# Optimization experiments

Hardware: AMD Instinct MI355X
Metric: run time of the kernel (lower is better)

The kernel has to match this reference:

```python
import jax, jax.numpy as jnp
import numpy as np

L1_PENALTY = 0.01
RHO = 5.0
N_ITERS = 100  # fixed iteration count standing in for max_iter=2000 w/ tol
EPS = 1e-12


def _normalize(x):
    # matches torch.nn.functional.normalize(dim=1, eps=1e-12)
    n = jnp.linalg.norm(x, axis=-1, keepdims=True)
    return x / jnp.maximum(n, EPS)


def _admm_nnlasso(D, Y, lam, rho, n_iters):
    """Batched nonnegative Lasso via ADMM.
    Solves per-row: min_w 0.5*||D^T w - y||^2 + lam*||w||_1, w >= 0.
    D: [c, d] dictionary, Y: [B, d] targets. Returns W: [B, c].
    x-update uses Woodbury: (A^T A + rho I)^{-1} b = (b - A^T (G + rho I)^{-1} A b)/rho
    with A = D^T, G = A A^T = D^T D ([d, d], d=512 -> cheap Cholesky).
    """
    d = D.shape[1]
    G = D.T @ D + rho * jnp.eye(d, dtype=D.dtype)  # [d, d]
    cf = jax.scipy.linalg.cho_factor(G)
    Aty = Y @ D.T  # [B, c] = A^T y batched
    thr = lam / rho

    def step(carry, _):
        z, u = carry
        b = Aty + rho * (z - u)               # [B, c]
        s = jax.scipy.linalg.cho_solve(cf, (b @ D).T).T  # [B, d]
        x = (b - s @ D.T) / rho               # [B, c]
        z_new = jnp.maximum(x + u - thr, 0.0)  # nonneg soft-threshold
        u_new = u + x - z_new
        return (z_new, u_new), None

    z0 = jnp.zeros_like(Aty)
    (z, _), _ = jax.lax.scan(step, (z0, z0), None, length=n_iters)
    return z


def setup_inputs() -> dict:
    key = jax.random.key(0)
    k1, k2, k3, k4 = jax.random.split(key, 4)
    B, C, Dm = 1024, 10000, 512
    image = jax.random.normal(k1, (B, Dm), dtype=jnp.float32)
    text = jax.random.normal(k2, (B, Dm), dtype=jnp.float32)
    image_mean = 0.1 * jax.random.normal(k3, (Dm,), dtype=jnp.float32)
    dictionary = jax.random.normal(k4, (C, Dm), dtype=jnp.float32)
    dictionary = dictionary / jnp.linalg.norm(dictionary, axis=1, keepdims=True)
    return {"image": image, "text": text, "image_mean": image_mean,
            "dictionary": dictionary}


def reference(image, text, image_mean, dictionary):
    # encode_image
    img = _normalize(image)
    centered = _normalize(img - image_mean)
    weights = _admm_nnlasso(dictionary, centered, L1_PENALTY, RHO, N_ITERS)
    recon = weights @ dictionary           # [B, d]
    recon = _normalize(recon)
    recon = _normalize(recon + image_mean)
    # encode_text (decomp_text=False -> just normalize)
    txt = _normalize(text)
    return recon, txt
```

## Files before the change

### kernel.cpp

```cpp
#include <hip/hip_runtime.h>
#include <cstddef>
#include <cstdint>

#define BDIM  1024
#define DM    512
#define CREAL 10000
#define CP    10112
#define KSPL  16
#define RHOC  5.0f
#define THRC  (0.01f/5.0f)
#define NIT   100
#define NSIT  12

typedef float f32x4 __attribute__((ext_vector_type(4)));
typedef _Float16 f16x8 __attribute__((ext_vector_type(8)));
typedef _Float16 f16x4 __attribute__((ext_vector_type(4)));
typedef unsigned int u32x4 __attribute__((ext_vector_type(4)));


__device__ __forceinline__ f16x8 scl6(f16x8 v) {
    f16x8 r;
#pragma unroll
    for (int i = 0; i < 8; i++) r[i] = v[i] * (_Float16)0.015625f;
    return r;
}

__device__ __forceinline__ void absfold(f16x8& h8, f16x8& l8) {
    u32x4 h = __builtin_bit_cast(u32x4, h8);
    u32x4 l = __builtin_bit_cast(u32x4, l8);
    u32x4 m = h & 0x80008000u;
    h8 = __builtin_bit_cast(f16x8, h ^ m);
    l8 = __builtin_bit_cast(f16x8, l ^ m);
}

__device__ __forceinline__ void relufold(f16x8& h8, f16x8& l8) {
#pragma unroll
    for (int e = 0; e < 8; e++) {
        bool p = h8[e] > (_Float16)0;
        if (!p) { h8[e] = (_Float16)0; l8[e] = (_Float16)0; }
    }
}

__device__ __forceinline__ size_t psidx(int row, int col) {
    return ((size_t)(row >> 4) * (CP >> 5) + (size_t)(col >> 5)) * 512
         + (size_t)((((col >> 3) & 3) * 16 + (row & 15)) * 8 + (col & 7));
}

__device__ __forceinline__ void dma16(const _Float16* g, _Float16* l) {
    __builtin_amdgcn_global_load_lds(
        (const __attribute__((address_space(1))) void*)g,
        (__attribute__((address_space(3))) void*)l, 16, 0, 0);
}

__device__ __forceinline__ float blk_sum256(float v) {
    __shared__ float sb[4];
#pragma unroll
    for (int o = 32; o; o >>= 1) v += __shfl_down(v, o, 64);
    int lane = threadIdx.x & 63, w = threadIdx.x >> 6;
    __syncthreads();
    if (lane == 0) sb[w] = v;
    __syncthreads();
    return sb[0] + sb[1] + sb[2] + sb[3];
}

__global__ __launch_bounds__(256) void knorm_rows(const float* __restrict__ X,
                                                  float* __restrict__ out) {
    int row = blockIdx.x, t = threadIdx.x;
    int off = row * DM + t * 2;
    float2 v = *(const float2*)(X + off);
    float ss = blk_sum256(v.x * v.x + v.y * v.y);
    float inv = 1.0f / fmaxf(sqrtf(ss), 1e-12f);
    float2 o = {v.x * inv, v.y * inv};
    *(float2*)(out + off) = o;
}

__global__ __launch_bounds__(256) void kprep_Y(const float* __restrict__ img,
                                               const float* __restrict__ mean,
                                               float* __restrict__ Y) {
    int row = blockIdx.x, t = threadIdx.x;
    int off = row * DM + t * 2;
    float2 v = *(const float2*)(img + off);
    float ss = blk_sum256(v.x * v.x + v.y * v.y);
    float inv = 1.0f / fmaxf(sqrtf(ss), 1e-12f);
    float2 mm = *(const float2*)(mean + t * 2);
    float tx = v.x * inv - mm.x, ty = v.y * inv - mm.y;
    float ss2 = blk_sum256(tx * tx + ty * ty);
    float inv2 = 1.0f / fmaxf(sqrtf(ss2), 1e-12f);
    float2 o = {tx * inv2, ty * inv2};
    *(float2*)(Y + off) = o;
}

__global__ __launch_bounds__(256) void ktrs(const float* __restrict__ in,
                                            float* __restrict__ out32,
                                            _Float16* __restrict__ oH,
                                            _Float16* __restrict__ oL,
                                            int Rvalid, int Cin, int Rout) {
    __shared__ float tile[64][65];
    int r0 = blockIdx.x * 64;
    int c0 = blockIdx.y * 64;
    int t = threadIdx.x;
    int ri = r0 + (t >> 2);
    int cc = (t & 3) * 16;
#pragma unroll
    for (int q = 0; q < 4; ++q) {
        float4 v = {0.f, 0.f, 0.f, 0.f};
        if (ri < Rvalid) v = *(const float4*)(in + (size_t)ri * Cin + c0 + cc + q * 4);
        *(float4*)&tile[t >> 2][cc + q * 4] = v;
    }
    __syncthreads();
    int oc = c0 + (t >> 2);
    int orr = r0 + (t & 3) * 16;
    _Float16 hv[16], lv[16];
#pragma unroll
    for (int q = 0; q < 16; ++q) {
        float v = tile[(t & 3) * 16 + q][t >> 2];
        _Float16 h = (_Float16)v;
        _Float16 l = (_Float16)((v - (float)h) * 64.f);
        hv[q] = h; lv[q] = l;
        if (out32) out32[(size_t)oc * Rout + orr + q] = (float)h + (float)l * 0.015625f;
    }
    int rt = oc >> 4, rin = oc & 15;
    int kt = orr >> 5;
    int kq0 = (orr >> 3) & 3;
    size_t base = ((size_t)rt * (Rout >> 5) + kt) * 512;
    *(f16x8*)(oH + base + (size_t)(kq0 * 16 + rin) * 8)       = *(f16x8*)&hv[0];
    *(f16x8*)(oH + base + (size_t)((kq0 + 1) * 16 + rin) * 8) = *(f16x8*)&hv[8];
    *(f16x8*)(oL + base + (size_t)(kq0 * 16 + rin) * 8)       = *(f16x8*)&lv[0];
    *(f16x8*)(oL + base + (size_t)((kq0 + 1) * 16 + rin) * 8) = *(f16x8*)&lv[8];
}

__global__ void kcsum(const float* __restrict__ Dt, float* __restrict__ csum) {
    int n = blockIdx.x, t = threadIdx.x;
    float s = 0.f;
    for (int k = t; k < CP; k += 64) s += Dt[(size_t)n * CP + k];
#pragma unroll
    for (int o = 32; o; o >>= 1) s += __shfl_down(s, o, 64);
    if (t == 0) csum[n] = s;
}

__global__ __launch_bounds__(256) void kG(const float* __restrict__ Dt,
                                          float* __restrict__ G) {
    __shared__ float As[32][68];
    __shared__ float Bs[32][68];
    int tid = threadIdx.x;
    int j0 = blockIdx.x * 64, i0 = blockIdx.y * 64;
    int tn = (tid & 15) * 4, tm = (tid >> 4) * 4;
    float acc[4][4];
#pragma unroll
    for (int i = 0; i < 4; i++)
#pragma unroll
        for (int j = 0; j < 4; j++) acc[i][j] = 0.f;
    for (int k0 = 0; k0 < CP; k0 += 32) {
        __syncthreads();
#pragma unroll
        for (int p = 0; p < 2; ++p) {
            int idx = tid + p * 256;
            int row = idx >> 3, kv = (idx & 7) << 2;
            float4 va = *(const float4*)(Dt + (size_t)(i0 + row) * CP + k0 + kv);
            As[kv + 0][row] = va.x; As[kv + 1][row] = va.y;
            As[kv + 2][row] = va.z; As[kv + 3][row] = va.w;
            float4 vb = *(const float4*)(Dt + (size_t)(j0 + row) * CP + k0 + kv);
            Bs[kv + 0][row] = vb.x; Bs[kv + 1][row] = vb.y;
            Bs[kv + 2][row] = vb.z; Bs[kv + 3][row] = vb.w;
        }
        __syncthreads();
#pragma unroll
        for (int k = 0; k < 32; ++k) {
            float4 a4 = *(const float4*)&As[k][tm];
            float4 b4 = *(const float4*)&Bs[k][tn];
            float af[4] = {a4.x, a4.y, a4.z, a4.w};
            float bf[4] = {b4.x, b4.y, b4.z, b4.w};
#pragma unroll
            for (int i = 0; i < 4; i++)
#pragma unroll
                for (int j = 0; j < 4; j++) acc[i][j] = fmaf(af[i], bf[j], acc[i][j]);
        }
    }
#pragma unroll
    for (int i = 0; i < 4; i++)
#pragma unroll
        for (int j = 0; j < 4; j++) {
            int gi = i0 + tm + i, gj = j0 + tn + j;
            G[gi * DM + gj] = acc[i][j] + ((gi == gj) ? RHOC : 0.f);
        }
}

__global__ void krow_abssum(const float* __restrict__ G, float* __restrict__ gmax) {
    int row = blockIdx.x, t = threadIdx.x;
    float s = 0.f;
    for (int j = t; j < DM; j += 64) s += fabsf(G[row * DM + j]);
#pragma unroll
    for (int o = 32; o; o >>= 1) s += __shfl_down(s, o, 64);
    if (t == 0) atomicMax((int*)gmax, __float_as_int(s));
}

__global__ void kinit_X0(const float* __restrict__ gmax, float* __restrict__ X) {
    int idx = blockIdx.x * 256 + threadIdx.x;
    int i = idx >> 9, j = idx & 511;
    X[idx] = (i == j) ? (1.0f / gmax[0]) : 0.0f;
}

__global__ __launch_bounds__(256) void kgemm_ns_T(const float* __restrict__ G,
                                                  const float* __restrict__ X,
                                                  float* __restrict__ T) {
    __shared__ float As[32][68];
    __shared__ float Bs[32][68];
    int tid = threadIdx.x;
    int n0 = blockIdx.x * 64, m0 = blockIdx.y * 64;
    int tn = (tid & 15) * 4, tm = (tid >> 4) * 4;
    float acc[4][4];
#pragma unroll
    for (int i = 0; i < 4; i++)
#pragma unroll
        for (int j = 0; j < 4; j++) acc[i][j] = 0.f;
    for (int k0 = 0; k0 < DM; k0 += 32) {
        __syncthreads();
#pragma unroll
        for (int p = 0; p < 2; ++p) {
            int idx = tid + p * 256;
            {
                int row = idx >> 3, kv = (idx & 7) << 2;
                float4 v = *(const float4*)(G + (m0 + row) * DM + k0 + kv);
                As[kv + 0][row] = v.x; As[kv + 1][row] = v.y;
                As[kv + 2][row] = v.z; As[kv + 3][row] = v.w;
            }
            {
                int r = idx >> 4, cv = (idx & 15) << 2;
                *(float4*)&Bs[r][cv] = *(const float4*)(X + (k0 + r) * DM + n0 + cv);
            }
        }
        __syncthreads();
#pragma unroll
        for (int k = 0; k < 32; ++k) {
            float4 a4 = *(const float4*)&As[k][tm];
            float4 b4 = *(const float4*)&Bs[k][tn];
            float af[4] = {a4.x, a4.y, a4.z, a4.w};
            float bf[4] = {b4.x, b4.y, b4.z, b4.w};
#pragma unroll
            for (int i = 0; i < 4; i++)
#pragma unroll
                for (int j = 0; j < 4; j++) acc[i][j] = fmaf(af[i], bf[j], acc[i][j]);
        }
    }
#pragma unroll
    for (int i = 0; i < 4; i++) {
        float4 o = {acc[i][0], acc[i][1], acc[i][2], acc[i][3]};
        *(float4*)(T + (m0 + tm + i) * DM + n0 + tn) = o;
    }
}

__global__ __launch_bounds__(256) void kgemm_ns_X(const float* __restrict__ Xo,
                                                  const float* __restrict__ T,
                                                  float* __restrict__ Xn) {
    __shared__ float As[32][68];
    __shared__ float Bs[32][68];
    int tid = threadIdx.x;
    int n0 = blockIdx.x * 64, m0 = blockIdx.y * 64;
    int tn = (tid & 15) * 4, tm = (tid >> 4) * 4;
    float acc[4][4];
#pragma unroll
    for (int i = 0; i < 4; i++)
#pragma unroll
        for (int j = 0; j < 4; j++) acc[i][j] = 0.f;
    for (int k0 = 0; k0 < DM; k0 += 32) {
        __syncthreads();
#pragma unroll
        for (int p = 0; p < 2; ++p) {
            int idx = tid + p * 256;
            {
                int row = idx >> 3, kv = (idx & 7) << 2;
                float4 v = *(const float4*)(Xo + (m0 + row) * DM + k0 + kv);
                As[kv + 0][row] = v.x; As[kv + 1][row] = v.y;
                As[kv + 2][row] = v.z; As[kv + 3][row] = v.w;
            }
            {
                int r = idx >> 4, cv = (idx & 15) << 2;
                *(float4*)&Bs[r][cv] = *(const float4*)(T + (k0 + r) * DM + n0 + cv);
            }
        }
        __syncthreads();
#pragma unroll
        for (int k = 0; k < 32; ++k) {
            float4 a4 = *(const float4*)&As[k][tm];
            float4 b4 = *(const float4*)&Bs[k][tn];
            float af[4] = {a4.x, a4.y, a4.z, a4.w};
            float bf[4] = {b4.x, b4.y, b4.z, b4.w};
#pragma unroll
            for (int i = 0; i < 4; i++)
#pragma unroll
                for (int j = 0; j < 4; j++) acc[i][j] = fmaf(af[i], bf[j], acc[i][j]);
        }
    }
#pragma unroll
    for (int i = 0; i < 4; i++) {
        int base = (m0 + tm + i) * DM + n0 + tn;
        float4 xo = *(const float4*)(Xo + base);
        float4 o = {2.f * xo.x - acc[i][0], 2.f * xo.y - acc[i][1],
                    2.f * xo.z - acc[i][2], 2.f * xo.w - acc[i][3]};
        *(float4*)(Xn + base) = o;
    }
}

template <int MODE>
__global__ __launch_bounds__(256) void kgemm_nn64(const float* __restrict__ A,
                                                  const float* __restrict__ B,
                                                  float* __restrict__ out32,
                                                  _Float16* __restrict__ oA) {
    __shared__ float As[32][68];
    __shared__ float Bs[32][68];
    int tid = threadIdx.x;
    int n0 = blockIdx.x * 64, m0 = blockIdx.y * 64;
    int tn = (tid & 15) * 4, tm = (tid >> 4) * 4;
    float acc[4][4];
#pragma unroll
    for (int i = 0; i < 4; i++)
#pragma unroll
        for (int j = 0; j < 4; j++) acc[i][j] = 0.f;
    for (int k0 = 0; k0 < DM; k0 += 32) {
        __syncthreads();
#pragma unroll
        for (int p = 0; p < 2; ++p) {
            int idx = tid + p * 256;
            {
                int row = idx >> 3, kv = (idx & 7) << 2;
                float4 v = *(const float4*)(A + (size_t)(m0 + row) * DM + k0 + kv);
                As[kv + 0][row] = v.x; As[kv + 1][row] = v.y;
                As[kv + 2][row] = v.z; As[kv + 3][row] = v.w;
            }
            {
                int r = idx >> 4, cv = (idx & 15) << 2;
                *(float4*)&Bs[r][cv] = *(const float4*)(B + (size_t)(k0 + r) * CP + n0 + cv);
            }
        }
        __syncthreads();
#pragma unroll
        for (int k = 0; k < 32; ++k) {
            float4 a4 = *(const float4*)&As[k][tm];
            float4 b4 = *(const float4*)&Bs[k][tn];
            float af[4] = {a4.x, a4.y, a4.z, a4.w};
            float bf[4] = {b4.x, b4.y, b4.z, b4.w};
#pragma unroll
            for (int i = 0; i < 4; i++)
#pragma unroll
                for (int j = 0; j < 4; j++) acc[i][j] = fmaf(af[i], bf[j], acc[i][j]);
        }
    }
#pragma unroll
    for (int i = 0; i < 4; i++)
#pragma unroll
        for (int j = 0; j < 4; j++) {
            size_t idx = (size_t)(m0 + tm + i) * CP + n0 + tn + j;
            if (MODE == 0) out32[idx] = acc[i][j];
            else           oA[idx] = (_Float16)(acc[i][j] * 0.2f * 64.f);
        }
}

__global__ __launch_bounds__(256) void kgemm_aD(const float* __restrict__ Yb,
                                                const float* __restrict__ G,
                                                const float* __restrict__ csum,
                                                float* __restrict__ aD) {
    __shared__ float As[32][68];
    __shared__ float Bs[32][68];
    int tid = threadIdx.x;
    int n0 = blockIdx.x * 64, m0 = blockIdx.y * 64;
    int tn = (tid & 15) * 4, tm = (tid >> 4) * 4;
    float acc[4][4];
#pragma unroll
    for (int i = 0; i < 4; i++)
#pragma unroll
        for (int j = 0; j < 4; j++) acc[i][j] = 0.f;
    for (int k0 = 0; k0 < DM; k0 += 32) {
        __syncthreads();
#pragma unroll
        for (int p = 0; p < 2; ++p) {
            int idx = tid + p * 256;
            {
                int row = idx >> 3, kv = (idx & 7) << 2;
                float4 v = *(const float4*)(Yb + (size_t)(m0 + row) * DM + k0 + kv);
                As[kv + 0][row] = v.x; As[kv + 1][row] = v.y;
                As[kv + 2][row] = v.z; As[kv + 3][row] = v.w;
            }
            {
                int r = idx >> 4, cv = (idx & 15) << 2;
                *(float4*)&Bs[r][cv] = *(const float4*)(G + (k0 + r) * DM + n0 + cv);
            }
        }
        __syncthreads();
#pragma unroll
        for (int k = 0; k < 32; ++k) {
            float4 a4 = *(const float4*)&As[k][tm];
            float4 b4 = *(const float4*)&Bs[k][tn];
            float af[4] = {a4.x, a4.y, a4.z, a4.w};
            float bf[4] = {b4.x, b4.y, b4.z, b4.w};
#pragma unroll
            for (int i = 0; i < 4; i++)
#pragma unroll
                for (int j = 0; j < 4; j++) acc[i][j] = fmaf(af[i], bf[j], acc[i][j]);
        }
    }
    float4 c4 = *(const float4*)(csum + n0 + tn);
#pragma unroll
    for (int i = 0; i < 4; i++) {
        int base = (m0 + tm + i) * DM + n0 + tn;
        float4 y4 = *(const float4*)(Yb + base);
        float4 o = {acc[i][0] * 0.2f - y4.x - THRC * c4.x,
                    acc[i][1] * 0.2f - y4.y - THRC * c4.y,
                    acc[i][2] * 0.2f - y4.z - THRC * c4.z,
                    acc[i][3] * 0.2f - y4.w - THRC * c4.w};
        *(float4*)(aD + base) = o;
    }
}

__global__ void kinit_s(_Float16* __restrict__ SHp, _Float16* __restrict__ SLp) {
    size_t i = ((size_t)blockIdx.x * 256 + threadIdx.x) * 8;
    _Float16 h = (_Float16)(-THRC);
    _Float16 l = (_Float16)((-THRC - (float)h) * 64.f);
    f16x8 hv, lv;
#pragma unroll
    for (int e = 0; e < 8; e++) { hv[e] = h; lv[e] = l; }
    *(f16x8*)(SHp + i) = hv;
    *(f16x8*)(SLp + i) = lv;
}


__device__ __forceinline__ void stage2(_Float16* __restrict__ sab,
                                       const _Float16* __restrict__ AHp,
                                       const _Float16* __restrict__ ALp,
                                       const _Float16* __restrict__ BHp,
                                       const _Float16* __restrict__ BLp,
                                       int sp, int mtbB, int ntbB, int ktA, int ktB,
                                       int wvu, int lane) {
#pragma unroll
    for (int k = 0; k < 4; ++k) {
        const int c = wvu * 4 + k;
        const int t = (c >> 1) & 7;
        const int p = c & 1;
        const _Float16* gp;
        if (c < 16) gp = (p ? ALp : AHp) + ((size_t)(mtbB + t) * ktA + sp) * 512 + (size_t)lane * 8;
        else        gp = (p ? BLp : BHp) + ((size_t)(ntbB + t) * ktB + sp) * 512 + (size_t)lane * 8;
        dma16(gp, sab + (size_t)c * 512);
    }
}

template <int FOLD>
__device__ __forceinline__ void compute8(const _Float16* __restrict__ sab,
                                         int wm, int wn, int lane,
                                         f32x4 (&acc)[4][2]) {
    const int ta = wm >> 4;
    const int tb = wn >> 4;
    f16x8 bh[2], bl[2], bs_[2];
#pragma unroll
    for (int j = 0; j < 2; ++j) {
        const _Float16* p = sab + 8192 + (size_t)(tb + j) * 1024 + (size_t)lane * 8;
        bh[j] = *(const f16x8*)p;
        bl[j] = *(const f16x8*)(p + 512);
        bs_[j] = scl6(bh[j]);
    }
    f16x8 ah[4], al[4], as_[4];
#pragma unroll
    for (int i = 0; i < 4; ++i) {
        const _Float16* p = sab + (size_t)(ta + i) * 1024 + (size_t)lane * 8;
        ah[i] = *(const f16x8*)p;
        al[i] = *(const f16x8*)(p + 512);
    }
#pragma unroll
    for (int i = 0; i < 4; ++i) {
        if (FOLD == 0) absfold(ah[i], al[i]);
        else if (FOLD == 1) relufold(ah[i], al[i]);
        as_[i] = scl6(ah[i]);
    }
#pragma unroll
    for (int i = 0; i < 4; ++i)
#pragma unroll
        for (int j = 0; j < 2; ++j) {
            acc[i][j] = __builtin_amdgcn_mfma_f32_16x16x32_f16(ah[i],  bh[j], acc[i][j], 0, 0, 0);
            acc[i][j] = __builtin_amdgcn_mfma_f32_16x16x32_f16(as_[i], bl[j], acc[i][j], 0, 0, 0);
            acc[i][j] = __builtin_amdgcn_mfma_f32_16x16x32_f16(al[i],  bs_[j], acc[i][j], 0, 0, 0);
        }
}

template <int MODE>
__global__ __launch_bounds__(512, 4) void kg1f(const _Float16* __restrict__ SHp,
                                               const _Float16* __restrict__ SLp,
                                               const _Float16* __restrict__ DHs,
                                               const _Float16* __restrict__ DLs,
                                               float* __restrict__ Qp) {
    __shared__ _Float16 sAB[2][16384];
    const int raw = blockIdx.x;
    const int xcd = raw & 7;
    const int r   = raw >> 3;
    const int ks  = xcd * 2 + (r & 1);
    const int q   = r >> 1;
    const int mb  = q >> 2, nb = q & 3;
    const int n0 = nb * 128, m0 = mb * 128;
    const int tid = threadIdx.x;
    const int lane = tid & 63;
    const int wvu = tid >> 6;
    const int wm = (wvu >> 2) * 64;
    const int wn = (wvu & 3) * 32;
    f32x4 acc[4][2] = {};

    const int steps = CP / 32;
    const int per = (steps + KSPL - 1) / KSPL;
    int s0 = ks * per;
    int s1 = s0 + per; if (s1 > steps) s1 = steps;

    const int mtbB = m0 >> 4;
    const int ntbB = n0 >> 4;
    const int KT = CP / 32;

    stage2(sAB[0], SHp, SLp, DHs, DLs, s0, mtbB, ntbB, KT, KT, wvu, lane);
    __syncthreads();

    for (int sp = s0; sp < s1; sp += 2) {
        stage2(sAB[1], SHp, SLp, DHs, DLs, sp + 1, mtbB, ntbB, KT, KT, wvu, lane);
        compute8<MODE>(sAB[0], wm, wn, lane, acc);
        __syncthreads();
        if (sp + 2 < s1)
            stage2(sAB[0], SHp, SLp, DHs, DLs, sp + 2, mtbB, ntbB, KT, KT, wvu, lane);
        compute8<MODE>(sAB[1], wm, wn, lane, acc);
        __syncthreads();
    }

    float* outp = Qp + (size_t)ks * (BDIM * DM);
    const int r0 = (lane >> 4) * 4, c0l = lane & 15;
#pragma unroll
    for (int i = 0; i < 4; i++)
#pragma unroll
        for (int v = 0; v < 4; v++) {
            int row = m0 + wm + i * 16 + r0 + v;
#pragma unroll
            for (int j = 0; j < 2; j++)
                outp[(size_t)row * DM + n0 + wn + j * 16 + c0l] = acc[i][j][v];
        }
}

template <int ADD>
__global__ void kredf(const float* __restrict__ Qp, const float* __restrict__ aD,
                      float* __restrict__ out32, _Float16* __restrict__ QH,
                      _Float16* __restrict__ QL) {
    size_t b = ((size_t)blockIdx.x * 256 + threadIdx.x) * 4;
    float4 s = {0.f, 0.f, 0.f, 0.f};
    if (ADD) s = *(const float4*)(aD + b);
#pragma unroll
    for (int qq = 0; qq < KSPL; qq++) {
        float4 t = *(const float4*)(Qp + (size_t)qq * (BDIM * DM) + b);
        s.x += t.x; s.y += t.y; s.z += t.z; s.w += t.w;
    }
    if (ADD) {
        int row = (int)(b >> 9), col = (int)(b & 511);
        size_t t0 = ((size_t)(row >> 4) * 16 + (size_t)(col >> 5)) * 512
                  + (size_t)((((col >> 3) & 3) * 16 + (row & 15)) * 8 + (col & 7));
        float sv[4] = {s.x, s.y, s.z, s.w};
        f16x4 h4, l4;
#pragma unroll
        for (int e = 0; e < 4; e++) {
            _Float16 h = (_Float16)sv[e];
            h4[e] = h;
            l4[e] = (_Float16)((sv[e] - (float)h) * 64.f);
        }
        *(f16x4*)(QH + t0) = h4;
        *(f16x4*)(QL + t0) = l4;
    } else {
        *(float4*)(out32 + b) = s;
    }
}

__global__ __launch_bounds__(512, 4) void kg2f(const _Float16* __restrict__ QH,
                                               const _Float16* __restrict__ QL,
                                               const _Float16* __restrict__ EHs,
                                               const _Float16* __restrict__ ELs,
                                               const _Float16* __restrict__ AH,
                                               _Float16* __restrict__ SHp,
                                               _Float16* __restrict__ SLp) {
    __shared__ _Float16 sAB[2][16384];
    const int raw = blockIdx.x;
    const int g = raw & 7;
    const int q = raw >> 3;
    const int mb = q & 7, jj = q >> 3;
    const int nb = g * 10 + jj;
    if (nb >= 79) return;
    const int n0 = nb * 128, m0 = mb * 128;
    const int tid = threadIdx.x;
    const int lane = tid & 63;
    const int wvu = tid >> 6;
    const int wm = (wvu >> 2) * 64;
    const int wn = (wvu & 3) * 32;
    const int mtbB = m0 >> 4;
    const int ntbB = n0 >> 4;
    const int KT = DM / 32;
    f32x4 acc[4][2] = {};

    stage2(sAB[0], QH, QL, EHs, ELs, 0, mtbB, ntbB, KT, KT, wvu, lane);
    __syncthreads();

    for (int kk = 0; kk < KT; kk += 2) {
        stage2(sAB[1], QH, QL, EHs, ELs, kk + 1, mtbB, ntbB, KT, KT, wvu, lane);
        compute8<2>(sAB[0], wm, wn, lane, acc);
        __syncthreads();
        if (kk + 2 < KT)
            stage2(sAB[0], QH, QL, EHs, ELs, kk + 2, mtbB, ntbB, KT, KT, wvu, lane);
        compute8<2>(sAB[1], wm, wn, lane, acc);
        __syncthreads();
    }

    const int r0 = (lane >> 4) * 4, c0l = lane & 15;
#pragma unroll
    for (int i = 0; i < 4; i++)
#pragma unroll
        for (int v = 0; v < 4; v++) {
            int row = m0 + wm + i * 16 + r0 + v;
#pragma unroll
            for (int j = 0; j < 2; j++) {
                int col = n0 + wn + j * 16 + c0l;
                size_t idx = (size_t)row * CP + col;
                size_t ps = psidx(row, col);
                float a = (float)AH[idx] * 0.015625f;
                float sold = (float)SHp[ps] + (float)SLp[ps] * 0.015625f;
                float z = fmaxf(sold, 0.f);
                float pn = a + z - acc[i][j][v];
                float sn = pn - THRC;
                _Float16 h = (_Float16)sn;
                SHp[ps] = h;
                SLp[ps] = (_Float16)((sn - (float)h) * 64.f);
            }
        }
}

__global__ __launch_bounds__(256) void kfinal(const float* __restrict__ Qf,
                                              const float* __restrict__ mean,
                                              float* __restrict__ out) {
    int row = blockIdx.x, t = threadIdx.x;
    int off = row * DM + t * 2;
    float2 qv = *(const float2*)(Qf + off);
    float rx = qv.x, ry = qv.y;
    float ss = blk_sum256(rx * rx + ry * ry);
    float inv = 1.0f / fmaxf(sqrtf(ss), 1e-12f);
    rx *= inv; ry *= inv;
    float2 mm = *(const float2*)(mean + t * 2);
    rx += mm.x; ry += mm.y;
    float ss2 = blk_sum256(rx * rx + ry * ry);
    float inv2 = 1.0f / fmaxf(sqrtf(ss2), 1e-12f);
    float2 o = {rx * inv2, ry * inv2};
    *(float2*)(out + off) = o;
}

extern "C" void kernel_launch(void* const* d_in, const int* in_sizes, int n_in,
                              void* d_out, int out_size, void* d_ws, size_t ws_size,
                              hipStream_t stream) {
    const float* image = (const float*)d_in[0];
    const float* text  = (const float*)d_in[1];
    const float* mean  = (const float*)d_in[2];
    const float* D     = (const float*)d_in[3];
    float* out = (float*)d_out;
    float* ws = (float*)d_ws;

    const size_t PLH = (size_t)DM * CP;
    float* aD   = ws;
    _Float16* QH = (_Float16*)(ws + 524288);
    _Float16* QL = QH + (size_t)BDIM * DM;
    _Float16* DHs = (_Float16*)(ws + 1048576);
    _Float16* DLs = DHs + PLH;
    _Float16* EHs = DLs + PLH;
    _Float16* ELs = EHs + PLH;
    _Float16* AH  = ELs + PLH;
    _Float16* SH  = AH + (size_t)BDIM * CP;
    _Float16* SL  = SH + (size_t)BDIM * CP;
    float* Qp   = (float*)(SL + (size_t)BDIM * CP);
    float* csum = Qp + (size_t)KSPL * BDIM * DM;
    float* gmax = csum + 512;
    float* Dt32 = (float*)SH;
    float* G    = Dt32 + (size_t)DM * CP;
    float* Xa   = G + 262144;
    float* Xb   = Xa + 262144;
    float* Tns  = Xb + 262144;
    float* Y    = Tns + 262144;
    float* Et32 = (float*)AH;

    knorm_rows<<<BDIM, 256, 0, stream>>>(text, out + (size_t)BDIM * DM);
    kprep_Y<<<BDIM, 256, 0, stream>>>(image, mean, Y);
    ktrs<<<dim3(CP / 64, DM / 64), 256, 0, stream>>>(D, Dt32, DHs, DLs, CREAL, DM, CP);
    kcsum<<<DM, 64, 0, stream>>>(Dt32, csum);
    kG<<<dim3(8, 8), 256, 0, stream>>>(Dt32, G);
    (void)hipMemsetAsync(gmax, 0, 4, stream);
    krow_abssum<<<DM, 64, 0, stream>>>(G, gmax);
    kinit_X0<<<DM * DM / 256, 256, 0, stream>>>(gmax, Xa);
    float* xc = Xa;
    float* xn = Xb;
    for (int it = 0; it < NSIT; ++it) {
        kgemm_ns_T<<<dim3(8, 8), 256, 0, stream>>>(G, xc, Tns);
        kgemm_ns_X<<<dim3(8, 8), 256, 0, stream>>>(xc, Tns, xn);
        float* tmp = xc; xc = xn; xn = tmp;
    }
    float* Ginv = xc;
    kgemm_nn64<0><<<dim3(CP / 64, DM / 64), 256, 0, stream>>>(Ginv, Dt32, Et32, nullptr);
    ktrs<<<dim3(DM / 64, CP / 64), 256, 0, stream>>>(Et32, nullptr, EHs, ELs, DM, CP, DM);
    kgemm_nn64<1><<<dim3(CP / 64, BDIM / 64), 256, 0, stream>>>(Y, Dt32, nullptr, AH);
    kgemm_aD<<<dim3(DM / 64, BDIM / 64), 256, 0, stream>>>(Y, G, csum, aD);
    kinit_s<<<(int)((size_t)BDIM * CP / 8 / 256), 256, 0, stream>>>(SH, SL);

    for (int it = 0; it < NIT; ++it) {
        kg1f<0><<<512, 512, 0, stream>>>(SH, SL, DHs, DLs, Qp);
        kredf<1><<<BDIM * DM / 1024, 256, 0, stream>>>(Qp, aD, nullptr, QH, QL);
        kg2f<<<640, 512, 0, stream>>>(QH, QL, EHs, ELs, AH, SH, SL);
    }

    kg1f<1><<<512, 512, 0, stream>>>(SH, SL, DHs, DLs, Qp);
    kredf<0><<<BDIM * DM / 1024, 256, 0, stream>>>(Qp, nullptr, aD, nullptr, nullptr);
    kfinal<<<BDIM, 256, 0, stream>>>(aD, mean, out);
}
```

Before: 11.33 ms.

## Store A in packed tile layout and vectorize epilogue via LDS transpose

The Aty-like matrix AH is now written in the same packed tile layout (psidx) as the split-fp16 state. The update epilogue stages the MFMA accumulators through LDS so each lane handles 8 contiguous elements, giving 16-byte vector loads and stores of AH, SHp and SLp in place of scattered 2-byte accesses. MFMA sections are also wrapped in s_setprio to favour matrix issue. The cost is extra LDS traffic and a reuse of the staging buffer after the main loop.

```diff
diff --git a/kernel.cpp b/kernel.cpp
--- a/kernel.cpp
+++ b/kernel.cpp
@@ -349,9 +349,9 @@
     for (int i = 0; i < 4; i++)
 #pragma unroll
         for (int j = 0; j < 4; j++) {
-            size_t idx = (size_t)(m0 + tm + i) * CP + n0 + tn + j;
-            if (MODE == 0) out32[idx] = acc[i][j];
-            else           oA[idx] = (_Float16)(acc[i][j] * 0.2f * 64.f);
+            int row = m0 + tm + i, col = n0 + tn + j;
+            if (MODE == 0) out32[(size_t)row * CP + col] = acc[i][j];
+            else           oA[psidx(row, col)] = (_Float16)(acc[i][j] * 0.2f * 64.f);
         }
 }
 
@@ -469,6 +469,7 @@
         else if (FOLD == 1) relufold(ah[i], al[i]);
         as_[i] = scl6(ah[i]);
     }
+    __builtin_amdgcn_s_setprio(1);
 #pragma unroll
     for (int i = 0; i < 4; ++i)
 #pragma unroll
@@ -477,6 +478,7 @@
             acc[i][j] = __builtin_amdgcn_mfma_f32_16x16x32_f16(as_[i], bl[j], acc[i][j], 0, 0, 0);
             acc[i][j] = __builtin_amdgcn_mfma_f32_16x16x32_f16(al[i],  bs_[j], acc[i][j], 0, 0, 0);
         }
+    __builtin_amdgcn_s_setprio(0);
 }
 
 template <int MODE>
@@ -605,26 +607,38 @@
     }
 
     const int r0 = (lane >> 4) * 4, c0l = lane & 15;
-#pragma unroll
-    for (int i = 0; i < 4; i++)
-#pragma unroll
-        for (int v = 0; v < 4; v++) {
-            int row = m0 + wm + i * 16 + r0 + v;
-#pragma unroll
-            for (int j = 0; j < 2; j++) {
-                int col = n0 + wn + j * 16 + c0l;
-                size_t idx = (size_t)row * CP + col;
-                size_t ps = psidx(row, col);
-                float a = (float)AH[idx] * 0.015625f;
-                float sold = (float)SHp[ps] + (float)SLp[ps] * 0.015625f;
-                float z = fmaxf(sold, 0.f);
-                float pn = a + z - acc[i][j][v];
-                float sn = pn - THRC;
-                _Float16 h = (_Float16)sn;
-                SHp[ps] = h;
-                SLp[ps] = (_Float16)((sn - (float)h) * 64.f);
-            }
-        }
+    const int mtbA = (m0 + wm) >> 4;
+    const int ktb  = (n0 + wn) >> 5;
+#pragma unroll
+    for (int i = 0; i < 4; ++i) {
+        float* sT = (float*)(&sAB[i & 1][0]) + wvu * (16 * 36);
+#pragma unroll
+        for (int j = 0; j < 2; ++j)
+#pragma unroll
+            for (int v = 0; v < 4; ++v)
+                sT[(r0 + v) * 36 + j * 16 + c0l] = acc[i][j][v];
+        float e[8];
+        *(float4*)&e[0] = *(const float4*)&sT[(lane & 15) * 36 + (lane >> 4) * 8];
+        *(float4*)&e[4] = *(const float4*)&sT[(lane & 15) * 36 + (lane >> 4) * 8 + 4];
+        size_t base = ((size_t)(mtbA + i) * (CP >> 5) + ktb) * 512 + (size_t)lane * 8;
+        f16x8 ah8 = *(const f16x8*)(AH + base);
+        f16x8 sh8 = *(const f16x8*)(SHp + base);
+        f16x8 sl8 = *(const f16x8*)(SLp + base);
+        f16x8 nh, nl;
+#pragma unroll
+        for (int e8 = 0; e8 < 8; ++e8) {
+            float a = (float)ah8[e8] * 0.015625f;
+            float sold = (float)sh8[e8] + (float)sl8[e8] * 0.015625f;
+            float z = fmaxf(sold, 0.f);
+            float pn = a + z - e[e8];
+            float sn = pn - THRC;
+            _Float16 h = (_Float16)sn;
+            nh[e8] = h;
+            nl[e8] = (_Float16)((sn - (float)h) * 64.f);
+        }
+        *(f16x8*)(SHp + base) = nh;
+        *(f16x8*)(SLp + base) = nl;
+    }
 }
 
 __global__ __launch_bounds__(256) void kfinal(const float* __restrict__ Qf,
```

After: 9.524 ms. 16.0% less time.
